# Performance work log

Measured on AMD Instinct MI355X. Metric: run time of the kernel, lower is better.

## Reference

```python
import jax, jax.numpy as jnp
import numpy as np

EPS = 1e-12
LAMBDA = 0.5  # kernel['lambda'] for the binary kernel

D, H, Z = 3072, 1024, 32
BS, NN = 128, 32


def setup_inputs() -> dict:
    key = jax.random.key(0)
    ks = jax.random.split(key, 16)
    sc = lambda fan_in: 1.0 / np.sqrt(fan_in)
    inp = {
        "x_c": jax.random.normal(ks[0], (BS, D), jnp.float32),
        "x_nn": jax.random.normal(ks[1], (BS, NN, D), jnp.float32),
        # encoder params: D -> H -> H -> Z
        "We1": jax.random.normal(ks[2], (D, H), jnp.float32) * sc(D),
        "be1": jnp.zeros((H,), jnp.float32),
        "We2": jax.random.normal(ks[3], (H, H), jnp.float32) * sc(H),
        "be2": jnp.zeros((H,), jnp.float32),
        "We3": jax.random.normal(ks[4], (H, Z), jnp.float32) * sc(H),
        "be3": jnp.zeros((Z,), jnp.float32),
        # decoder params: Z -> H -> H -> D
        "Wd1": jax.random.normal(ks[5], (Z, H), jnp.float32) * sc(Z),
        "bd1": jnp.zeros((H,), jnp.float32),
        "Wd2": jax.random.normal(ks[6], (H, H), jnp.float32) * sc(H),
        "bd2": jnp.zeros((H,), jnp.float32),
        "Wd3": jax.random.normal(ks[7], (H, D), jnp.float32) * sc(H),
        "bd3": jnp.zeros((D,), jnp.float32),
    }
    return inp


def _mlp(x, W1, b1, W2, b2, W3, b3):
    h = jax.nn.relu(x @ W1 + b1)
    h = jax.nn.relu(h @ W2 + b2)
    return h @ W3 + b3


def reference(x_c, x_nn, We1, be1, We2, be2, We3, be3,
              Wd1, bd1, Wd2, bd2, Wd3, bd3):
    bs, num_nn, dim = x_nn.shape

    enc = lambda x: _mlp(x, We1, be1, We2, be2, We3, be3)
    dec = lambda z: _mlp(z, Wd1, bd1, Wd2, bd2, Wd3, bd3)

    z_c = enc(x_c)                                   # (bs, Z)
    z_dim = z_c.shape[1]
    z_nn = enc(x_nn.reshape(-1, dim)).reshape(bs, num_nn, z_dim)

    recon = dec(z_c)                                 # (bs, D)
    dz = z_nn - z_c[:, None, :]                      # (bs, nn, Z)
    v = dz.reshape(-1, z_dim)                        # (bs*nn, Z)
    inputs = jnp.broadcast_to(z_c[:, None, :], (bs, num_nn, z_dim)).reshape(-1, z_dim)

    # approx_order == 2: Jacobian-vector and Hessian-bilinear (dz^T H dz) via nested jvp
    jac_fn = lambda z: jax.jvp(dec, (z,), (v,))[1]   # J(z) dz, (bs*nn, D)
    jac, hess = jax.jvp(jac_fn, (inputs,), (v,))     # each (bs*nn, D)

    n_recon = recon[:, None, :] + (jac + 0.5 * hess).reshape(bs, num_nn, dim)

    n_loss = jnp.sum((x_nn - n_recon) ** 2, axis=2)  # ||.||^2, (bs, nn)

    # binary kernel: 1 where neighbor differs from center, lambda where identical
    dist = jnp.linalg.norm(x_c[:, None, :] - x_nn, axis=2)
    weights = jnp.where(dist > EPS, 1.0, LAMBDA)

    loss = jnp.mean(weights * n_loss)
    return loss
```

## Files before the change

kernel.cpp:

```cpp
#include <hip/hip_runtime.h>
#include <math.h>

#define D_DIM 3072
#define H_DIM 1024
#define Z_DIM 32
#define BATCH 128
#define NNEI 32
#define NROWS (BATCH * NNEI)
#define MENC (NROWS + BATCH)

typedef __attribute__((ext_vector_type(8))) short short8;
typedef __attribute__((ext_vector_type(4))) float f32x4;
typedef unsigned short ushortT;

__device__ __forceinline__ unsigned short f2bf(float f) {
  union { float f; unsigned int u; } v; v.f = f;
  unsigned int r = v.u + 0x7FFFu + ((v.u >> 16) & 1u);
  return (unsigned short)(r >> 16);
}
__device__ __forceinline__ float bf2f(unsigned short b) {
  union { unsigned int u; float f; } v; v.u = ((unsigned int)b) << 16;
  return v.f;
}

enum { EP_RELU = 0, EP_BIAS = 1, EP_PART = 2, EP_LOSS = 3 };

template <int MODE, int TN>
__global__ __launch_bounds__(256) __attribute__((amdgpu_waves_per_eu(1, 2)))
void gemm64(
    const ushortT* __restrict__ A, const ushortT* __restrict__ BT,
    const float* __restrict__ bias, ushortT* __restrict__ C,
    float* __restrict__ P, int M, int N, int K, int Ks,
    const ushortT* __restrict__ xa,
    const float* __restrict__ wrow,
    float* __restrict__ out) {
  constexpr int NF = TN / 32;

  __shared__ __align__(16) ushortT As[8192];
  __shared__ __align__(16) ushortT Bs[TN * 64];

  const int t = threadIdx.x;
  const int wave = t >> 6;
  const int lane = t & 63;
  const int quad = lane >> 4;
  const int lm = lane & 15;
  const int bm = blockIdx.y * 128;
  const int bn = blockIdx.x * TN;
  const int koff = blockIdx.z * Ks;
  const int wr = (wave >> 1) * 64;
  const int wc = (wave & 1) * (TN / 2);

  f32x4 acc[4][NF];
#pragma unroll
  for (int i = 0; i < 4; ++i)
#pragma unroll
    for (int j = 0; j < NF; ++j) acc[i][j] = (f32x4)0.f;

  const int a_r0 = (t >> 6) * 16 + (t & 15);
  const int a_q8 = ((t >> 4) & 3) * 8;
  const ushortT* ga = A + (size_t)(bm + a_r0) * K + koff + a_q8;
  const size_t aK64 = (size_t)64 * K;

  const ushortT* gb = nullptr;
  if (TN == 128) {
    gb = BT + (size_t)(bn + a_r0) * K + koff + a_q8;
  } else {
    const int b_r = ((t >> 6) & 1) * 16 + (t & 15);
    const int b_k = (t >> 7) * 32 + ((t >> 4) & 3) * 8;
    gb = BT + (size_t)(bn + b_r) * K + koff + b_k;
  }

  uint4 a0, a1, a2, a3, b0, b1 = {0,0,0,0}, b2 = {0,0,0,0}, b3 = {0,0,0,0};

#define LOADT(kk)                                               \
  {                                                             \
    const size_t o = (size_t)(kk) * 64;                         \
    a0 = *(const uint4*)(ga + o);                               \
    a1 = *(const uint4*)(ga + aK64 + o);                        \
    a2 = *(const uint4*)(ga + o + 32);                          \
    a3 = *(const uint4*)(ga + aK64 + o + 32);                   \
    b0 = *(const uint4*)(gb + o);                               \
    if (TN == 128) {                                            \
      b1 = *(const uint4*)(gb + aK64 + o);                      \
      b2 = *(const uint4*)(gb + o + 32);                        \
      b3 = *(const uint4*)(gb + aK64 + o + 32);                 \
    }                                                           \
  }
#define STORET()                                                \
  {                                                             \
    *(uint4*)&As[t * 8] = a0;                                   \
    *(uint4*)&As[t * 8 + 2048] = a1;                            \
    *(uint4*)&As[t * 8 + 4096] = a2;                            \
    *(uint4*)&As[t * 8 + 6144] = a3;                            \
    if (TN == 128) {                                            \
      *(uint4*)&Bs[t * 8] = b0;                                 \
      *(uint4*)&Bs[t * 8 + 2048] = b1;                          \
      *(uint4*)&Bs[t * 8 + 4096] = b2;                          \
      *(uint4*)&Bs[t * 8 + 6144] = b3;                          \
    } else {                                                    \
      *(uint4*)&Bs[t * 8] = b0;                                 \
    }                                                           \
  }

  const int nk = Ks / 64;
  LOADT(0);

  for (int k0 = 0; k0 < nk; ++k0) {
    __syncthreads();
    STORET();
    __syncthreads();
    if (k0 + 1 < nk) LOADT(k0 + 1);

#pragma unroll
    for (int kk = 0; kk < 2; ++kk) {
      const ushortT* arp = &As[kk * 4096 + (wr >> 4) * 512 + lane * 8];
      const ushortT* brp = (TN == 128)
          ? &Bs[kk * 4096 + (wc >> 4) * 512 + lane * 8]
          : &Bs[kk * 1024 + (wc >> 4) * 512 + lane * 8];
      short8 af[4], bf[NF];
#pragma unroll
      for (int mt = 0; mt < 4; ++mt) af[mt] = *(const short8*)(arp + mt * 512);
#pragma unroll
      for (int nt = 0; nt < NF; ++nt) bf[nt] = *(const short8*)(brp + nt * 512);
#pragma unroll
      for (int mt = 0; mt < 4; ++mt)
#pragma unroll
        for (int nt = 0; nt < NF; ++nt)
          acc[mt][nt] = __builtin_amdgcn_mfma_f32_16x16x32_bf16(af[mt], bf[nt], acc[mt][nt], 0, 0, 0);
    }
  }
#undef LOADT
#undef STORET

  if (MODE == EP_LOSS) {
    __shared__ float red[256];
    float lsum = 0.f;
#pragma unroll
    for (int mt = 0; mt < 4; ++mt) {
#pragma unroll
      for (int r = 0; r < 4; ++r) {
        const int row = bm + wr + mt * 16 + quad * 4 + r;
        const float w = wrow[row];
        const ushortT* xr = xa + (size_t)row * N;
        float rs = 0.f;
#pragma unroll
        for (int nt = 0; nt < NF; ++nt) {
          const int col = bn + wc + nt * 16 + lm;
          const float d = bf2f(xr[col]) - (acc[mt][nt][r] + bias[col]);
          rs = fmaf(d, d, rs);
        }
        lsum = fmaf(w, rs, lsum);
      }
    }
    __syncthreads();
    red[t] = lsum;
    __syncthreads();
    for (int st = 128; st > 0; st >>= 1) {
      if (t < st) red[t] += red[t + st];
      __syncthreads();
    }
    if (t == 0) atomicAdd(out, red[0] * (1.0f / (float)NROWS));
  } else if (MODE == EP_PART) {
#pragma unroll
    for (int mt = 0; mt < 4; ++mt)
#pragma unroll
      for (int r = 0; r < 4; ++r) {
        const int row = bm + wr + mt * 16 + quad * 4 + r;
#pragma unroll
        for (int nt = 0; nt < NF; ++nt) {
          const int col = bn + wc + nt * 16 + lm;
          P[((size_t)blockIdx.z * M + row) * N + col] = acc[mt][nt][r];
        }
      }
  } else {
#pragma unroll
    for (int mt = 0; mt < 4; ++mt)
#pragma unroll
      for (int r = 0; r < 4; ++r) {
        const int row = bm + wr + mt * 16 + quad * 4 + r;
#pragma unroll
        for (int nt = 0; nt < NF; ++nt) {
          const int col = bn + wc + nt * 16 + lm;
          float v = acc[mt][nt][r] + bias[col];
          if (MODE == EP_RELU) v = fmaxf(v, 0.f);
          C[(size_t)row * N + col] = f2bf(v);
        }
      }
  }
}

template <int MODE, int TN>
__global__ __launch_bounds__(256) __attribute__((amdgpu_waves_per_eu(1, 2)))
void gemm_sb(
    const ushortT* __restrict__ A, const ushortT* __restrict__ BT,
    const float* __restrict__ bias, ushortT* __restrict__ C,
    int M, int N, int K,
    const ushortT* __restrict__ xa, const float* __restrict__ wrow,
    float* __restrict__ out) {
  constexpr int NF = TN / 32;
  __shared__ __align__(16) ushortT As[4096];
  __shared__ __align__(16) ushortT Bs[TN * 32];

  const int t = threadIdx.x;
  const int wave = t >> 6;
  const int lane = t & 63;
  const int quad = lane >> 4;
  const int lm = lane & 15;
  const int bm = blockIdx.y * 128;
  const int bn = blockIdx.x * TN;
  const int wr = (wave >> 1) * 64;
  const int wc = (wave & 1) * (TN / 2);

  f32x4 acc[4][NF];
#pragma unroll
  for (int i = 0; i < 4; ++i)
#pragma unroll
    for (int j = 0; j < NF; ++j) acc[i][j] = (f32x4)0.f;

  const int a_r0 = (t >> 6) * 16 + (t & 15);
  const int a_q8 = ((t >> 4) & 3) * 8;
  const ushortT* ga0 = A + (size_t)(bm + a_r0) * K + a_q8;
  const ushortT* ga1 = ga0 + (size_t)64 * K;
  const ushortT* gb0 = BT + (size_t)(bn + a_r0) * K + a_q8;
  const ushortT* gb1 = gb0 + (size_t)64 * K;

  uint4 ra0 = *(const uint4*)ga0;
  uint4 ra1 = *(const uint4*)ga1;
  uint4 rb0 = *(const uint4*)gb0;
  uint4 rb1 = *(const uint4*)gb1;
  ga0 += 32; ga1 += 32; gb0 += 32; gb1 += 32;

  const ushortT* arp = As + (wr >> 4) * 512 + lane * 8;
  const ushortT* brp = Bs + (wc >> 4) * 512 + lane * 8;

  for (int k0 = 0; k0 < K; k0 += 32) {
    __syncthreads();
    *(uint4*)&As[t * 8] = ra0;
    *(uint4*)&As[t * 8 + 2048] = ra1;
    *(uint4*)&Bs[t * 8] = rb0;
    *(uint4*)&Bs[t * 8 + 2048] = rb1;
    __syncthreads();
    if (k0 + 32 < K) {
      ra0 = *(const uint4*)ga0;
      ra1 = *(const uint4*)ga1;
      rb0 = *(const uint4*)gb0;
      rb1 = *(const uint4*)gb1;
      ga0 += 32; ga1 += 32; gb0 += 32; gb1 += 32;
    }
    short8 af[4], bf[NF];
#pragma unroll
    for (int mt = 0; mt < 4; ++mt) af[mt] = *(const short8*)(arp + mt * 512);
#pragma unroll
    for (int nt = 0; nt < NF; ++nt) bf[nt] = *(const short8*)(brp + nt * 512);
#pragma unroll
    for (int mt = 0; mt < 4; ++mt)
#pragma unroll
      for (int nt = 0; nt < NF; ++nt)
        acc[mt][nt] = __builtin_amdgcn_mfma_f32_16x16x32_bf16(af[mt], bf[nt], acc[mt][nt], 0, 0, 0);
  }

#pragma unroll
  for (int mt = 0; mt < 4; ++mt)
#pragma unroll
    for (int r = 0; r < 4; ++r) {
      const int row = bm + wr + mt * 16 + quad * 4 + r;
#pragma unroll
      for (int nt = 0; nt < NF; ++nt) {
        const int col = bn + wc + nt * 16 + lm;
        float v = acc[mt][nt][r] + bias[col];
        if (MODE == EP_RELU) v = fmaxf(v, 0.f);
        C[(size_t)row * N + col] = f2bf(v);
      }
    }
}

template <int S>
__global__ __launch_bounds__(256) void reduce_lin(
    const float* __restrict__ P, const float* __restrict__ bias,
    ushortT* __restrict__ outp, int MN, int Nmask) {
  const int i4 = (blockIdx.x * 256 + threadIdx.x) * 4;
  if (i4 >= MN) return;
  float4 s = *(const float4*)(P + i4);
#pragma unroll
  for (int k = 1; k < S; ++k) {
    const float4 q = *(const float4*)(P + (size_t)k * MN + i4);
    s.x += q.x; s.y += q.y; s.z += q.z; s.w += q.w;
  }
  const float4 b = *(const float4*)(bias + (i4 & Nmask));
  ushort4 o;
  o.x = f2bf(s.x + b.x); o.y = f2bf(s.y + b.y);
  o.z = f2bf(s.z + b.z); o.w = f2bf(s.w + b.w);
  *(ushort4*)(outp + i4) = o;
}

__global__ __launch_bounds__(256) void mask_apply(
    const ushortT* __restrict__ U, ushortT* __restrict__ outp) {
  const int i4 = (blockIdx.x * 256 + threadIdx.x) * 4;
  const int r = i4 >> 10;
  const int c = i4 & 1023;
  ushort4 u = *(const ushort4*)(U + i4);
  ushort4 o;
  if (r < NROWS) {
    const ushort4 m = *(const ushort4*)(U + (((size_t)(NROWS + (r >> 5))) << 10) + c);
    o.x = ((short)m.x > 0) ? u.x : 0;
    o.y = ((short)m.y > 0) ? u.y : 0;
    o.z = ((short)m.z > 0) ? u.z : 0;
    o.w = ((short)m.w > 0) ? u.w : 0;
  } else {
    o.x = ((short)u.x > 0) ? u.x : 0;
    o.y = ((short)u.y > 0) ? u.y : 0;
    o.z = ((short)u.z > 0) ? u.z : 0;
    o.w = ((short)u.w > 0) ? u.w : 0;
  }
  *(ushort4*)(outp + i4) = o;
}

__global__ __launch_bounds__(256) void prep_kernel(
    const float* __restrict__ x_c, const float* __restrict__ x_nn,
    ushortT* __restrict__ A_enc, float* __restrict__ wbuf, float* __restrict__ out) {
  const int i = blockIdx.x;
  const int t = threadIdx.x;
  if (i < NROWS) {
    const float* src = x_nn + (size_t)i * D_DIM;
    const float* ctr = x_c + (size_t)(i >> 5) * D_DIM;
    ushortT* dst = A_enc + (size_t)i * D_DIM;
    float s = 0.f;
    for (int d = t * 4; d < D_DIM; d += 1024) {
      const float4 v = *(const float4*)(src + d);
      const float4 c = *(const float4*)(ctr + d);
      ushort4 o;
      o.x = f2bf(v.x); o.y = f2bf(v.y); o.z = f2bf(v.z); o.w = f2bf(v.w);
      *(ushort4*)(dst + d) = o;
      const float dx = v.x - c.x, dy = v.y - c.y, dz = v.z - c.z, dw = v.w - c.w;
      s += dx * dx + dy * dy + dz * dz + dw * dw;
    }
    __shared__ float red[256];
    red[t] = s;
    __syncthreads();
    for (int st = 128; st > 0; st >>= 1) {
      if (t < st) red[t] += red[t + st];
      __syncthreads();
    }
    if (t == 0) {
      wbuf[i] = (red[0] > 1e-24f) ? 1.0f : 0.5f;
      if (i == 0) out[0] = 0.f;
    }
  } else {
    const int r = i - NROWS;
    const float* src = x_c + (size_t)r * D_DIM;
    ushortT* dst = A_enc + (size_t)i * D_DIM;
    for (int d = t * 4; d < D_DIM; d += 1024) {
      const float4 v = *(const float4*)(src + d);
      ushort4 o;
      o.x = f2bf(v.x); o.y = f2bf(v.y); o.z = f2bf(v.z); o.w = f2bf(v.w);
      *(ushort4*)(dst + d) = o;
    }
  }
}

__global__ __launch_bounds__(256) void trans_all(
    const float* __restrict__ We1, const float* __restrict__ We2,
    const float* __restrict__ We3, const float* __restrict__ Wd1,
    const float* __restrict__ Wd2, const float* __restrict__ Wd3,
    ushortT* __restrict__ We1T, ushortT* __restrict__ We2T,
    ushortT* __restrict__ We3T, ushortT* __restrict__ Wd1T,
    ushortT* __restrict__ Wd2T, ushortT* __restrict__ Wd3T) {
  const int b = blockIdx.x;
  const float* W; ushortT* WT; int K, N, loc;
  if (b < 3072)      { W = We1; WT = We1T; K = 3072; N = 1024; loc = b; }
  else if (b < 4096) { W = We2; WT = We2T; K = 1024; N = 1024; loc = b - 3072; }
  else if (b < 4128) { W = We3; WT = We3T; K = 1024; N = 32;   loc = b - 4096; }
  else if (b < 4160) { W = Wd1; WT = Wd1T; K = 32;   N = 1024; loc = b - 4128; }
  else if (b < 5184) { W = Wd2; WT = Wd2T; K = 1024; N = 1024; loc = b - 4160; }
  else               { W = Wd3; WT = Wd3T; K = 1024; N = 3072; loc = b - 5184; }
  const int ntiles = N >> 5;
  const int n0 = (loc % ntiles) * 32;
  const int k0 = (loc / ntiles) * 32;
  __shared__ float tile[32][33];
  const int tx = threadIdx.x & 31;
  const int ty = threadIdx.x >> 5;
  for (int i = ty; i < 32; i += 8)
    tile[i][tx] = W[(size_t)(k0 + i) * N + n0 + tx];
  __syncthreads();
  for (int i = ty; i < 32; i += 8)
    WT[(size_t)(n0 + i) * K + k0 + tx] = f2bf(tile[tx][i]);
}

extern "C" void kernel_launch(void* const* d_in, const int* in_sizes, int n_in,
                              void* d_out, int out_size, void* d_ws, size_t ws_size,
                              hipStream_t stream) {
  const float* x_c = (const float*)d_in[0];
  const float* x_nn = (const float*)d_in[1];
  const float* We1 = (const float*)d_in[2];
  const float* be1 = (const float*)d_in[3];
  const float* We2 = (const float*)d_in[4];
  const float* be2 = (const float*)d_in[5];
  const float* We3 = (const float*)d_in[6];
  const float* be3 = (const float*)d_in[7];
  const float* Wd1 = (const float*)d_in[8];
  const float* bd1 = (const float*)d_in[9];
  const float* Wd2 = (const float*)d_in[10];
  const float* bd2 = (const float*)d_in[11];
  const float* Wd3 = (const float*)d_in[12];
  const float* bd3 = (const float*)d_in[13];
  float* out = (float*)d_out;

  char* p = (char*)d_ws;
  auto alloc = [&](size_t bytes) {
    char* r = p;
    p += (bytes + 255) & ~(size_t)255;
    return r;
  };
  ushortT* We1T = (ushortT*)alloc((size_t)H_DIM * D_DIM * 2);
  ushortT* We2T = (ushortT*)alloc((size_t)H_DIM * H_DIM * 2);
  ushortT* We3T = (ushortT*)alloc((size_t)Z_DIM * H_DIM * 2);
  ushortT* Wd1T = (ushortT*)alloc((size_t)H_DIM * Z_DIM * 2);
  ushortT* Wd2T = (ushortT*)alloc((size_t)H_DIM * H_DIM * 2);
  ushortT* Wd3T = (ushortT*)alloc((size_t)D_DIM * H_DIM * 2);
  ushortT* A_enc = (ushortT*)alloc((size_t)MENC * D_DIM * 2);
  ushortT* bufX = (ushortT*)alloc((size_t)MENC * H_DIM * 2);
  ushortT* bufY = (ushortT*)alloc((size_t)MENC * H_DIM * 2);
  ushortT* z = (ushortT*)alloc((size_t)MENC * Z_DIM * 2);
  float* Pz = (float*)alloc((size_t)8 * MENC * Z_DIM * 4);
  float* wbuf = (float*)alloc((size_t)NROWS * 4);

  const dim3 blk(256);
  const float* nofp = nullptr;
  const ushortT* nobf = nullptr;

  prep_kernel<<<dim3(MENC), blk, 0, stream>>>(x_c, x_nn, A_enc, wbuf, out);
  trans_all<<<dim3(8256), blk, 0, stream>>>(We1, We2, We3, Wd1, Wd2, Wd3,
                                            We1T, We2T, We3T, Wd1T, Wd2T, Wd3T);

  gemm64<EP_RELU, 128><<<dim3(8, 33, 1), blk, 0, stream>>>(
      A_enc, We1T, be1, bufX, nullptr, MENC, H_DIM, D_DIM, D_DIM, nobf, nofp, nullptr);
  gemm64<EP_RELU, 128><<<dim3(8, 33, 1), blk, 0, stream>>>(
      bufX, We2T, be2, bufY, nullptr, MENC, H_DIM, H_DIM, H_DIM, nobf, nofp, nullptr);
  gemm64<EP_PART, 32><<<dim3(1, 33, 8), blk, 0, stream>>>(
      bufY, We3T, nofp, nullptr, Pz, MENC, Z_DIM, H_DIM, H_DIM / 8, nobf, nofp, nullptr);
  reduce_lin<8><<<dim3((MENC * Z_DIM) / 1024), blk, 0, stream>>>(
      Pz, be3, z, MENC * Z_DIM, Z_DIM - 1);

  gemm_sb<EP_BIAS, 128><<<dim3(8, 33), blk, 0, stream>>>(
      z, Wd1T, bd1, bufX, MENC, H_DIM, Z_DIM, nobf, nofp, nullptr);
  mask_apply<<<dim3((MENC * H_DIM) / 1024), blk, 0, stream>>>(bufX, bufY);
  gemm64<EP_BIAS, 128><<<dim3(8, 33, 1), blk, 0, stream>>>(
      bufY, Wd2T, bd2, bufX, nullptr, MENC, H_DIM, H_DIM, H_DIM, nobf, nofp, nullptr);
  mask_apply<<<dim3((NROWS * H_DIM) / 1024), blk, 0, stream>>>(bufX, bufY);
  gemm64<EP_LOSS, 128><<<dim3(24, 32, 1), blk, 0, stream>>>(
      bufY, Wd3T, bd3, nullptr, nullptr, NROWS, D_DIM, H_DIM, H_DIM, A_enc, wbuf, out);
}
```

Measured before the change: 390.5 us.

## Use 128x64 tiles, XCD-aware block remap, and higher occupancy for hidden GEMMs

Adds a TN=64 tile variant to the GEMM kernels and launches the encoder and decoder hidden-layer GEMMs with it. This doubles the workgroup count from 264 to 528 so the 256 CUs are filled better. It also remaps linear block ids in a round-robin-by-8 pattern so neighbouring tiles land on the same XCD and share L2. It raises waves_per_eu to 2-4 for more latency hiding, at the cost of register pressure, which could cause spills, and of lower per-tile data reuse.

```diff
diff --git a/kernel.cpp b/kernel.cpp
--- a/kernel.cpp
+++ b/kernel.cpp
@@ -26,7 +26,7 @@
 enum { EP_RELU = 0, EP_BIAS = 1, EP_PART = 2, EP_LOSS = 3 };
 
 template <int MODE, int TN>
-__global__ __launch_bounds__(256) __attribute__((amdgpu_waves_per_eu(1, 2)))
+__global__ __launch_bounds__(256) __attribute__((amdgpu_waves_per_eu(2, 4)))
 void gemm64(
     const ushortT* __restrict__ A, const ushortT* __restrict__ BT,
     const float* __restrict__ bias, ushortT* __restrict__ C,
@@ -44,8 +44,13 @@
   const int lane = t & 63;
   const int quad = lane >> 4;
   const int lm = lane & 15;
-  const int bm = blockIdx.y * 128;
-  const int bn = blockIdx.x * TN;
+
+  int id = blockIdx.y * gridDim.x + blockIdx.x;
+  const int nwg = gridDim.x * gridDim.y;
+  if ((nwg & 7) == 0) id = (id & 7) * (nwg >> 3) + (id >> 3);
+  const int bm = (id / gridDim.x) * 128;
+  const int bn = (id % gridDim.x) * TN;
+
   const int koff = blockIdx.z * Ks;
   const int wr = (wave >> 1) * 64;
   const int wc = (wave & 1) * (TN / 2);
@@ -62,7 +67,7 @@
   const size_t aK64 = (size_t)64 * K;
 
   const ushortT* gb = nullptr;
-  if (TN == 128) {
+  if (TN >= 64) {
     gb = BT + (size_t)(bn + a_r0) * K + koff + a_q8;
   } else {
     const int b_r = ((t >> 6) & 1) * 16 + (t & 15);
@@ -84,6 +89,8 @@
       b1 = *(const uint4*)(gb + aK64 + o);                      \
       b2 = *(const uint4*)(gb + o + 32);                        \
       b3 = *(const uint4*)(gb + aK64 + o + 32);                 \
+    } else if (TN == 64) {                                      \
+      b1 = *(const uint4*)(gb + o + 32);                        \
     }                                                           \
   }
 #define STORET()                                                \
@@ -92,13 +99,13 @@
     *(uint4*)&As[t * 8 + 2048] = a1;                            \
     *(uint4*)&As[t * 8 + 4096] = a2;                            \
     *(uint4*)&As[t * 8 + 6144] = a3;                            \
+    *(uint4*)&Bs[t * 8] = b0;                                   \
     if (TN == 128) {                                            \
-      *(uint4*)&Bs[t * 8] = b0;                                 \
       *(uint4*)&Bs[t * 8 + 2048] = b1;                          \
       *(uint4*)&Bs[t * 8 + 4096] = b2;                          \
       *(uint4*)&Bs[t * 8 + 6144] = b3;                          \
-    } else {                                                    \
-      *(uint4*)&Bs[t * 8] = b0;                                 \
+    } else if (TN == 64) {                                      \
+      *(uint4*)&Bs[t * 8 + 2048] = b1;                          \
     }                                                           \
   }
 
@@ -114,9 +121,9 @@
 #pragma unroll
     for (int kk = 0; kk < 2; ++kk) {
       const ushortT* arp = &As[kk * 4096 + (wr >> 4) * 512 + lane * 8];
-      const ushortT* brp = (TN == 128)
-          ? &Bs[kk * 4096 + (wc >> 4) * 512 + lane * 8]
-          : &Bs[kk * 1024 + (wc >> 4) * 512 + lane * 8];
+      const ushortT* brp =
+          &Bs[(TN == 128 ? kk * 4096 : TN == 64 ? kk * 2048 : kk * 1024) +
+              (wc >> 4) * 512 + lane * 8];
       short8 af[4], bf[NF];
 #pragma unroll
       for (int mt = 0; mt < 4; ++mt) af[mt] = *(const short8*)(arp + mt * 512);
@@ -190,7 +197,7 @@
 }
 
 template <int MODE, int TN>
-__global__ __launch_bounds__(256) __attribute__((amdgpu_waves_per_eu(1, 2)))
+__global__ __launch_bounds__(256) __attribute__((amdgpu_waves_per_eu(2, 4)))
 void gemm_sb(
     const ushortT* __restrict__ A, const ushortT* __restrict__ BT,
     const float* __restrict__ bias, ushortT* __restrict__ C,
@@ -206,8 +213,13 @@
   const int lane = t & 63;
   const int quad = lane >> 4;
   const int lm = lane & 15;
-  const int bm = blockIdx.y * 128;
-  const int bn = blockIdx.x * TN;
+
+  int id = blockIdx.y * gridDim.x + blockIdx.x;
+  const int nwg = gridDim.x * gridDim.y;
+  if ((nwg & 7) == 0) id = (id & 7) * (nwg >> 3) + (id >> 3);
+  const int bm = (id / gridDim.x) * 128;
+  const int bn = (id % gridDim.x) * TN;
+
   const int wr = (wave >> 1) * 64;
   const int wc = (wave & 1) * (TN / 2);
 
@@ -227,7 +239,8 @@
   uint4 ra0 = *(const uint4*)ga0;
   uint4 ra1 = *(const uint4*)ga1;
   uint4 rb0 = *(const uint4*)gb0;
-  uint4 rb1 = *(const uint4*)gb1;
+  uint4 rb1 = {0, 0, 0, 0};
+  if (TN == 128) rb1 = *(const uint4*)gb1;
   ga0 += 32; ga1 += 32; gb0 += 32; gb1 += 32;
 
   const ushortT* arp = As + (wr >> 4) * 512 + lane * 8;
@@ -238,13 +251,13 @@
     *(uint4*)&As[t * 8] = ra0;
     *(uint4*)&As[t * 8 + 2048] = ra1;
     *(uint4*)&Bs[t * 8] = rb0;
-    *(uint4*)&Bs[t * 8 + 2048] = rb1;
+    if (TN == 128) *(uint4*)&Bs[t * 8 + 2048] = rb1;
     __syncthreads();
     if (k0 + 32 < K) {
       ra0 = *(const uint4*)ga0;
       ra1 = *(const uint4*)ga1;
       rb0 = *(const uint4*)gb0;
-      rb1 = *(const uint4*)gb1;
+      if (TN == 128) rb1 = *(const uint4*)gb1;
       ga0 += 32; ga1 += 32; gb0 += 32; gb1 += 32;
     }
     short8 af[4], bf[NF];
@@ -432,19 +445,19 @@
   trans_all<<<dim3(8256), blk, 0, stream>>>(We1, We2, We3, Wd1, Wd2, Wd3,
                                             We1T, We2T, We3T, Wd1T, Wd2T, Wd3T);
 
-  gemm64<EP_RELU, 128><<<dim3(8, 33, 1), blk, 0, stream>>>(
+  gemm64<EP_RELU, 64><<<dim3(16, 33, 1), blk, 0, stream>>>(
       A_enc, We1T, be1, bufX, nullptr, MENC, H_DIM, D_DIM, D_DIM, nobf, nofp, nullptr);
-  gemm64<EP_RELU, 128><<<dim3(8, 33, 1), blk, 0, stream>>>(
+  gemm64<EP_RELU, 64><<<dim3(16, 33, 1), blk, 0, stream>>>(
       bufX, We2T, be2, bufY, nullptr, MENC, H_DIM, H_DIM, H_DIM, nobf, nofp, nullptr);
   gemm64<EP_PART, 32><<<dim3(1, 33, 8), blk, 0, stream>>>(
       bufY, We3T, nofp, nullptr, Pz, MENC, Z_DIM, H_DIM, H_DIM / 8, nobf, nofp, nullptr);
   reduce_lin<8><<<dim3((MENC * Z_DIM) / 1024), blk, 0, stream>>>(
       Pz, be3, z, MENC * Z_DIM, Z_DIM - 1);
 
-  gemm_sb<EP_BIAS, 128><<<dim3(8, 33), blk, 0, stream>>>(
+  gemm_sb<EP_BIAS, 64><<<dim3(16, 33), blk, 0, stream>>>(
       z, Wd1T, bd1, bufX, MENC, H_DIM, Z_DIM, nobf, nofp, nullptr);
   mask_apply<<<dim3((MENC * H_DIM) / 1024), blk, 0, stream>>>(bufX, bufY);
-  gemm64<EP_BIAS, 128><<<dim3(8, 33, 1), blk, 0, stream>>>(
+  gemm64<EP_BIAS, 64><<<dim3(16, 33, 1), blk, 0, stream>>>(
       bufY, Wd2T, bd2, bufX, nullptr, MENC, H_DIM, H_DIM, H_DIM, nobf, nofp, nullptr);
   mask_apply<<<dim3((NROWS * H_DIM) / 1024), blk, 0, stream>>>(bufX, bufY);
   gemm64<EP_LOSS, 128><<<dim3(24, 32, 1), blk, 0, stream>>>(
```

New measurement: 410.2 us. 5.0% more time.

## Split-K the encoder and decoder GEMMs, remap workgroups, rewrite the small-K decoder GEMM

Applied to the files above, without the earlier changes.

The H-wide encoder and decoder GEMMs (8x33 = 264 blocks) now run as split-K partial GEMMs writing fp32 partials into a shared buffer, followed by reduce kernels that add bias and apply ReLU. This spreads the work over more workgroups to fill the CUs. The gemm64 and gemm_sb kernels also remap block IDs into 8 interleaved groups, and the occupancy hint changes to 4 waves per EU. The K=32 decoder-input GEMM becomes a single-stage load straight into LDS via global_load_lds with a 64-wide tile. The cost is extra fp32 partial traffic through global memory and extra reduce launches.

```diff
diff --git a/kernel.cpp b/kernel.cpp
--- a/kernel.cpp
+++ b/kernel.cpp
@@ -23,10 +23,26 @@
   return v.f;
 }
 
+__device__ __forceinline__ void gl16(const ushortT* g, ushortT* l) {
+  typedef __attribute__((address_space(1))) const void gvoid;
+  typedef __attribute__((address_space(3))) void lvoid;
+  __builtin_amdgcn_global_load_lds((gvoid*)(const void*)g, (lvoid*)(void*)l,
+                                   16, 0, 0);
+}
+typedef __attribute__((address_space(3))) const ushortT lds_cus;
+__device__ __forceinline__ short8 ldsr(const ushortT* p) {
+  short8 r;
+  asm volatile("ds_read_b128 %0, %1" : "=v"(r) : "v"((lds_cus*)p));
+  return r;
+}
+#define BAR() asm volatile("s_barrier" ::: "memory")
+#define VM0() asm volatile("s_waitcnt vmcnt(0)" ::: "memory")
+#define LGKM0() asm volatile("s_waitcnt lgkmcnt(0)" ::: "memory")
+
 enum { EP_RELU = 0, EP_BIAS = 1, EP_PART = 2, EP_LOSS = 3 };
 
 template <int MODE, int TN>
-__global__ __launch_bounds__(256) __attribute__((amdgpu_waves_per_eu(1, 2)))
+__global__ __launch_bounds__(256) __attribute__((amdgpu_waves_per_eu(4)))
 void gemm64(
     const ushortT* __restrict__ A, const ushortT* __restrict__ BT,
     const float* __restrict__ bias, ushortT* __restrict__ C,
@@ -44,8 +60,13 @@
   const int lane = t & 63;
   const int quad = lane >> 4;
   const int lm = lane & 15;
-  const int bm = blockIdx.y * 128;
-  const int bn = blockIdx.x * TN;
+
+  int id = blockIdx.y * gridDim.x + blockIdx.x;
+  const int nwg = gridDim.x * gridDim.y;
+  if ((nwg & 7) == 0) id = (id & 7) * (nwg >> 3) + (id >> 3);
+  const int bm = (id / gridDim.x) * 128;
+  const int bn = (id % gridDim.x) * TN;
+
   const int koff = blockIdx.z * Ks;
   const int wr = (wave >> 1) * 64;
   const int wc = (wave & 1) * (TN / 2);
@@ -190,8 +211,7 @@
 }
 
 template <int MODE, int TN>
-__global__ __launch_bounds__(256) __attribute__((amdgpu_waves_per_eu(1, 2)))
-void gemm_sb(
+__global__ __launch_bounds__(256) void gemm_sb(
     const ushortT* __restrict__ A, const ushortT* __restrict__ BT,
     const float* __restrict__ bias, ushortT* __restrict__ C,
     int M, int N, int K,
@@ -206,58 +226,51 @@
   const int lane = t & 63;
   const int quad = lane >> 4;
   const int lm = lane & 15;
-  const int bm = blockIdx.y * 128;
-  const int bn = blockIdx.x * TN;
+
+  int id = blockIdx.y * gridDim.x + blockIdx.x;
+  const int nwg = gridDim.x * gridDim.y;
+  if ((nwg & 7) == 0) id = (id & 7) * (nwg >> 3) + (id >> 3);
+  const int bm = (id / gridDim.x) * 128;
+  const int bn = (id % gridDim.x) * TN;
+
   const int wr = (wave >> 1) * 64;
   const int wc = (wave & 1) * (TN / 2);
-
-  f32x4 acc[4][NF];
-#pragma unroll
-  for (int i = 0; i < 4; ++i)
-#pragma unroll
-    for (int j = 0; j < NF; ++j) acc[i][j] = (f32x4)0.f;
 
   const int a_r0 = (t >> 6) * 16 + (t & 15);
   const int a_q8 = ((t >> 4) & 3) * 8;
   const ushortT* ga0 = A + (size_t)(bm + a_r0) * K + a_q8;
-  const ushortT* ga1 = ga0 + (size_t)64 * K;
   const ushortT* gb0 = BT + (size_t)(bn + a_r0) * K + a_q8;
-  const ushortT* gb1 = gb0 + (size_t)64 * K;
-
-  uint4 ra0 = *(const uint4*)ga0;
-  uint4 ra1 = *(const uint4*)ga1;
-  uint4 rb0 = *(const uint4*)gb0;
-  uint4 rb1 = *(const uint4*)gb1;
-  ga0 += 32; ga1 += 32; gb0 += 32; gb1 += 32;
+
+  ushortT* asw = &As[wave * 512];
+  ushortT* bsw = &Bs[wave * 512];
+  gl16(ga0, asw);
+  gl16(ga0 + (size_t)64 * K, asw + 2048);
+  gl16(gb0, bsw);
+  if (TN == 128) gl16(gb0 + (size_t)64 * K, bsw + 2048);
+  VM0();
+  BAR();
+
+  f32x4 acc[4][NF];
+#pragma unroll
+  for (int i = 0; i < 4; ++i)
+#pragma unroll
+    for (int j = 0; j < NF; ++j) acc[i][j] = (f32x4)0.f;
 
   const ushortT* arp = As + (wr >> 4) * 512 + lane * 8;
   const ushortT* brp = Bs + (wc >> 4) * 512 + lane * 8;
-
-  for (int k0 = 0; k0 < K; k0 += 32) {
-    __syncthreads();
-    *(uint4*)&As[t * 8] = ra0;
-    *(uint4*)&As[t * 8 + 2048] = ra1;
-    *(uint4*)&Bs[t * 8] = rb0;
-    *(uint4*)&Bs[t * 8 + 2048] = rb1;
-    __syncthreads();
-    if (k0 + 32 < K) {
-      ra0 = *(const uint4*)ga0;
-      ra1 = *(const uint4*)ga1;
-      rb0 = *(const uint4*)gb0;
-      rb1 = *(const uint4*)gb1;
-      ga0 += 32; ga1 += 32; gb0 += 32; gb1 += 32;
-    }
-    short8 af[4], bf[NF];
-#pragma unroll
-    for (int mt = 0; mt < 4; ++mt) af[mt] = *(const short8*)(arp + mt * 512);
-#pragma unroll
-    for (int nt = 0; nt < NF; ++nt) bf[nt] = *(const short8*)(brp + nt * 512);
-#pragma unroll
-    for (int mt = 0; mt < 4; ++mt)
-#pragma unroll
-      for (int nt = 0; nt < NF; ++nt)
-        acc[mt][nt] = __builtin_amdgcn_mfma_f32_16x16x32_bf16(af[mt], bf[nt], acc[mt][nt], 0, 0, 0);
-  }
+  short8 af[4], bf[NF];
+#pragma unroll
+  for (int mt = 0; mt < 4; ++mt) af[mt] = ldsr(arp + mt * 512);
+#pragma unroll
+  for (int nt = 0; nt < NF; ++nt) bf[nt] = ldsr(brp + nt * 512);
+  LGKM0();
+  __builtin_amdgcn_sched_barrier(0);
+#pragma unroll
+  for (int mt = 0; mt < 4; ++mt)
+#pragma unroll
+    for (int nt = 0; nt < NF; ++nt)
+      acc[mt][nt] = __builtin_amdgcn_mfma_f32_16x16x32_bf16(
+          af[mt], bf[nt], acc[mt][nt], 0, 0, 0);
 
 #pragma unroll
   for (int mt = 0; mt < 4; ++mt)
@@ -274,7 +287,7 @@
     }
 }
 
-template <int S>
+template <int S, int RELU>
 __global__ __launch_bounds__(256) void reduce_lin(
     const float* __restrict__ P, const float* __restrict__ bias,
     ushortT* __restrict__ outp, int MN, int Nmask) {
@@ -287,9 +300,13 @@
     s.x += q.x; s.y += q.y; s.z += q.z; s.w += q.w;
   }
   const float4 b = *(const float4*)(bias + (i4 & Nmask));
+  float vx = s.x + b.x, vy = s.y + b.y, vz = s.z + b.z, vw = s.w + b.w;
+  if (RELU) {
+    vx = fmaxf(vx, 0.f); vy = fmaxf(vy, 0.f);
+    vz = fmaxf(vz, 0.f); vw = fmaxf(vw, 0.f);
+  }
   ushort4 o;
-  o.x = f2bf(s.x + b.x); o.y = f2bf(s.y + b.y);
-  o.z = f2bf(s.z + b.z); o.w = f2bf(s.w + b.w);
+  o.x = f2bf(vx); o.y = f2bf(vy); o.z = f2bf(vz); o.w = f2bf(vw);
   *(ushort4*)(outp + i4) = o;
 }
 
@@ -421,7 +438,7 @@
   ushortT* bufX = (ushortT*)alloc((size_t)MENC * H_DIM * 2);
   ushortT* bufY = (ushortT*)alloc((size_t)MENC * H_DIM * 2);
   ushortT* z = (ushortT*)alloc((size_t)MENC * Z_DIM * 2);
-  float* Pz = (float*)alloc((size_t)8 * MENC * Z_DIM * 4);
+  float* Pbig = (float*)alloc((size_t)4 * MENC * H_DIM * 4);
   float* wbuf = (float*)alloc((size_t)NROWS * 4);
 
   const dim3 blk(256);
@@ -432,21 +449,34 @@
   trans_all<<<dim3(8256), blk, 0, stream>>>(We1, We2, We3, Wd1, Wd2, Wd3,
                                             We1T, We2T, We3T, Wd1T, Wd2T, Wd3T);
 
-  gemm64<EP_RELU, 128><<<dim3(8, 33, 1), blk, 0, stream>>>(
-      A_enc, We1T, be1, bufX, nullptr, MENC, H_DIM, D_DIM, D_DIM, nobf, nofp, nullptr);
-  gemm64<EP_RELU, 128><<<dim3(8, 33, 1), blk, 0, stream>>>(
-      bufX, We2T, be2, bufY, nullptr, MENC, H_DIM, H_DIM, H_DIM, nobf, nofp, nullptr);
+  gemm64<EP_PART, 128><<<dim3(8, 33, 4), blk, 0, stream>>>(
+      A_enc, We1T, nofp, nullptr, Pbig, MENC, H_DIM, D_DIM, D_DIM / 4,
+      nobf, nofp, nullptr);
+  reduce_lin<4, 1><<<dim3((MENC * H_DIM) / 1024), blk, 0, stream>>>(
+      Pbig, be1, bufX, MENC * H_DIM, H_DIM - 1);
+
+  gemm64<EP_PART, 128><<<dim3(8, 33, 2), blk, 0, stream>>>(
+      bufX, We2T, nofp, nullptr, Pbig, MENC, H_DIM, H_DIM, H_DIM / 2,
+      nobf, nofp, nullptr);
+  reduce_lin<2, 1><<<dim3((MENC * H_DIM) / 1024), blk, 0, stream>>>(
+      Pbig, be2, bufY, MENC * H_DIM, H_DIM - 1);
+
   gemm64<EP_PART, 32><<<dim3(1, 33, 8), blk, 0, stream>>>(
-      bufY, We3T, nofp, nullptr, Pz, MENC, Z_DIM, H_DIM, H_DIM / 8, nobf, nofp, nullptr);
-  reduce_lin<8><<<dim3((MENC * Z_DIM) / 1024), blk, 0, stream>>>(
-      Pz, be3, z, MENC * Z_DIM, Z_DIM - 1);
-
-  gemm_sb<EP_BIAS, 128><<<dim3(8, 33), blk, 0, stream>>>(
+      bufY, We3T, nofp, nullptr, Pbig, MENC, Z_DIM, H_DIM, H_DIM / 8,
+      nobf, nofp, nullptr);
+  reduce_lin<8, 0><<<dim3((MENC * Z_DIM) / 1024), blk, 0, stream>>>(
+      Pbig, be3, z, MENC * Z_DIM, Z_DIM - 1);
+
+  gemm_sb<EP_BIAS, 64><<<dim3(16, 33), blk, 0, stream>>>(
       z, Wd1T, bd1, bufX, MENC, H_DIM, Z_DIM, nobf, nofp, nullptr);
   mask_apply<<<dim3((MENC * H_DIM) / 1024), blk, 0, stream>>>(bufX, bufY);
-  gemm64<EP_BIAS, 128><<<dim3(8, 33, 1), blk, 0, stream>>>(
-      bufY, Wd2T, bd2, bufX, nullptr, MENC, H_DIM, H_DIM, H_DIM, nobf, nofp, nullptr);
+  gemm64<EP_PART, 128><<<dim3(8, 33, 2), blk, 0, stream>>>(
+      bufY, Wd2T, nofp, nullptr, Pbig, MENC, H_DIM, H_DIM, H_DIM / 2,
+      nobf, nofp, nullptr);
+  reduce_lin<2, 0><<<dim3((MENC * H_DIM) / 1024), blk, 0, stream>>>(
+      Pbig, bd2, bufX, MENC * H_DIM, H_DIM - 1);
   mask_apply<<<dim3((NROWS * H_DIM) / 1024), blk, 0, stream>>>(bufX, bufY);
   gemm64<EP_LOSS, 128><<<dim3(24, 32, 1), blk, 0, stream>>>(
-      bufY, Wd3T, bd3, nullptr, nullptr, NROWS, D_DIM, H_DIM, H_DIM, A_enc, wbuf, out);
-}
+      bufY, Wd3T, bd3, nullptr, nullptr, NROWS, D_DIM, H_DIM, H_DIM,
+      A_enc, wbuf, out);
+}
```

Result: slower. 408.8 us (+4.7%).
